# Kernel tuning notes

Hardware: AMD Instinct MI355X
Metric: run time of the kernel (lower is better)

## Reference

```python
import jax, jax.numpy as jnp
import numpy as np


def setup_inputs() -> dict:
    key = jax.random.key(0)
    k1, k2 = jax.random.split(key)
    B, H, W, D, C = 2, 128, 128, 128, 4
    image = jax.random.normal(k1, (B, H, W, D, C), dtype=jnp.float32)
    # multiplicative warp field in [0,1) keeps sample coords inside the volume
    transformation = jax.random.uniform(k2, (B, H, W, D, 3), dtype=jnp.float32)
    return {"image": image, "transformation": transformation}


def _make_grid(OH, OW, OD):
    # matches tf.meshgrid(x_lin, y_lin, z_lin) with default 'xy' indexing:
    # each output has shape (OH, OW, OD); stacked last-dim order (x, y, z)
    xl = jnp.linspace(-1.0, 1.0, OW)
    yl = jnp.linspace(-1.0, 1.0, OH)
    zl = jnp.linspace(-1.0, 1.0, OD)
    xc, yc, zc = jnp.meshgrid(xl, yl, zl, indexing="xy")
    return jnp.stack([xc, yc, zc], axis=-1)  # (OH, OW, OD, 3)


def _trilerp_one(img, coords):
    """img: (H, W, D, C); coords: (OH, OW, OD, 3) in [-1, 1]-style space."""
    H, W, D, C = img.shape
    x = 0.5 * (coords[..., 0] + 1.0) * W
    y = 0.5 * (coords[..., 1] + 1.0) * H
    z = 0.5 * (coords[..., 2] + 1.0) * D

    x0 = jnp.floor(x).astype(jnp.int32)
    y0 = jnp.floor(y).astype(jnp.int32)
    z0 = jnp.floor(z).astype(jnp.int32)
    x1 = jnp.clip(x0 + 1, 0, W - 1)
    y1 = jnp.clip(y0 + 1, 0, H - 1)
    z1 = jnp.clip(z0 + 1, 0, D - 1)
    x0 = jnp.clip(x0, 0, W - 1)
    y0 = jnp.clip(y0, 0, H - 1)
    z0 = jnp.clip(z0, 0, D - 1)

    # weights use the CLIPPED upper corners, as in the original
    dx = x1.astype(x.dtype) - x
    dy = y1.astype(y.dtype) - y
    dz = z1.astype(z.dtype) - z

    def g(yy, xx, zz):
        return img[yy, xx, zz]  # (OH, OW, OD, C) gather

    w = lambda a: a[..., None]
    out = (
        w(dz * dx * dy) * g(y0, x0, z0)
        + w(dz * dx * (1 - dy)) * g(y1, x0, z0)
        + w(dz * (1 - dx) * dy) * g(y0, x1, z0)
        + w(dz * (1 - dx) * (1 - dy)) * g(y1, x1, z0)
        + w((1 - dz) * dx * dy) * g(y0, x0, z1)
        + w((1 - dz) * dx * (1 - dy)) * g(y1, x0, z1)
        + w((1 - dz) * (1 - dx) * dy) * g(y0, x1, z1)
        + w((1 - dz) * (1 - dx) * (1 - dy)) * g(y1, x1, z1)
    )
    return out


def reference(image, transformation):
    # image: (B, H, W, D, C); transformation: (B, OH, OW, OD, 3)
    OH, OW, OD = transformation.shape[1:4]
    grid = _make_grid(OH, OW, OD)              # (OH, OW, OD, 3)
    coords = transformation * grid             # elementwise warp, as in source
    return jax.vmap(_trilerp_one, in_axes=(0, 0))(image, coords)
```

## Files before the change

kernel.cpp:

```cpp
#include <hip/hip_runtime.h>
#include <hip/hip_fp16.h>


typedef float f4 __attribute__((ext_vector_type(4)));
typedef unsigned int u32;
typedef u32 u4v __attribute__((ext_vector_type(4), aligned(8)));

__device__ inline float2 h2f(u32 b) {
    __half2 h = __builtin_bit_cast(__half2, b);
    return __half22float2(h);
}

__global__ __launch_bounds__(256) void cvt_kernel(
    const f4* __restrict__ img, uint2* __restrict__ himg)
{
    int idx = blockIdx.x * 256 + threadIdx.x;
    f4 v = img[idx];
    __half2 lo = __floats2half2_rn(v.x, v.y);
    __half2 hi = __floats2half2_rn(v.z, v.w);
    himg[idx] = make_uint2(__builtin_bit_cast(u32, lo), __builtin_bit_cast(u32, hi));
}

__global__ __launch_bounds__(256) void st3d_h_kernel(
    const u32* __restrict__ himg,
    const float* __restrict__ trans,
    f4* __restrict__ out)
{
    int bid = blockIdx.x;
    int q   = bid & 7;
    int n   = bid >> 3;
    int b   = n >> 10;
    int m   = ((n & 1023) << 8) | threadIdx.x;

    int kp = m & 63;
    int jp = (m >> 6) & 63;
    int ip = m >> 12;

    int qi = (q >> 2) & 1;
    int qj = (q >> 1) & 1;
    int qk = q & 1;

    int ipe = qi ? ip : (63 - ip);
    int i = (qi << 6) + ipe;
    int j = (qj << 6) + jp;
    int k = (qk << 6) + kp;

    int idx = (((b << 7) | i) << 14) | (j << 7) | k;

    const float step = 2.0f / 127.0f;
    float gx = -1.0f + step * (float)j;
    float gy = -1.0f + step * (float)i;
    float gz = -1.0f + step * (float)k;

    const float* t = trans + (size_t)idx * 3;
    float tx = __builtin_nontemporal_load(t + 0);
    float ty = __builtin_nontemporal_load(t + 1);
    float tz = __builtin_nontemporal_load(t + 2);

    float x = (tx * gx + 1.0f) * 64.0f;
    float y = (ty * gy + 1.0f) * 64.0f;
    float z = (tz * gz + 1.0f) * 64.0f;

    int x0 = (int)floorf(x);
    int y0 = (int)floorf(y);
    int z0 = (int)floorf(z);
    int x1 = min(max(x0 + 1, 0), 127);
    int y1 = min(max(y0 + 1, 0), 127);
    int z1 = min(max(z0 + 1, 0), 127);
    x0 = min(max(x0, 0), 127);
    y0 = min(max(y0, 0), 127);
    z0 = min(max(z0, 0), 127);

    float dx = (float)x1 - x;
    float dy = (float)y1 - y;
    float dz = (float)z1 - z;
    float ex = 1.0f - dx;
    float ey = 1.0f - dy;
    float ez = 1.0f - dz;

    int zb = min(z0, 126);
    int i0 = z0 - zb;
    int i1 = z1 - zb;

    int bb  = b << 21;
    int ry0 = bb + (y0 << 14);
    int ry1 = bb + (y1 << 14);
    int cx0 = x0 << 7;
    int cx1 = x1 << 7;

    const u4v* p0 = (const u4v*)(himg + (size_t)(ry0 + cx0 + zb) * 2);
    const u4v* p1 = (const u4v*)(himg + (size_t)(ry1 + cx0 + zb) * 2);
    const u4v* p2 = (const u4v*)(himg + (size_t)(ry0 + cx1 + zb) * 2);
    const u4v* p3 = (const u4v*)(himg + (size_t)(ry1 + cx1 + zb) * 2);

    u4v d0 = *p0;
    u4v d1 = *p1;
    u4v d2 = *p2;
    u4v d3 = *p3;

    float wA0 = dz * dx * dy, wB0 = ez * dx * dy;
    float wA1 = dz * dx * ey, wB1 = ez * dx * ey;
    float wA2 = dz * ex * dy, wB2 = ez * ex * dy;
    float wA3 = dz * ex * ey, wB3 = ez * ex * ey;

    float ox = 0.f, oy = 0.f, oz = 0.f, ow = 0.f;

#define ACC(d, wA, wB)                                            \
    {                                                             \
        u32 a0 = i0 ? (d).z : (d).x;               \
        u32 a1 = i0 ? (d).w : (d).y;               \
        u32 b0 = i1 ? (d).z : (d).x;               \
        u32 b1 = i1 ? (d).w : (d).y;               \
        float2 fa0 = h2f(a0), fa1 = h2f(a1);                      \
        float2 fb0 = h2f(b0), fb1 = h2f(b1);                      \
        ox += (wA) * fa0.x + (wB) * fb0.x;                        \
        oy += (wA) * fa0.y + (wB) * fb0.y;                        \
        oz += (wA) * fa1.x + (wB) * fb1.x;                        \
        ow += (wA) * fa1.y + (wB) * fb1.y;                        \
    }

    ACC(d0, wA0, wB0)
    ACC(d1, wA1, wB1)
    ACC(d2, wA2, wB2)
    ACC(d3, wA3, wB3)
#undef ACC

    f4 o = {ox, oy, oz, ow};
    __builtin_nontemporal_store(o, &out[idx]);
}

__global__ __launch_bounds__(256) void st3d_kernel(
    const float* __restrict__ img,
    const float* __restrict__ trans,
    f4* __restrict__ out)
{
    int bid = blockIdx.x;
    int q   = bid & 7;
    int n   = bid >> 3;
    int b   = n >> 10;
    int m   = ((n & 1023) << 8) | threadIdx.x;

    int kp = m & 63;
    int jp = (m >> 6) & 63;
    int ip = m >> 12;

    int qi = (q >> 2) & 1;
    int qj = (q >> 1) & 1;
    int qk = q & 1;

    int ipe = qi ? ip : (63 - ip);
    int i = (qi << 6) + ipe;
    int j = (qj << 6) + jp;
    int k = (qk << 6) + kp;

    int idx = (((b << 7) | i) << 14) | (j << 7) | k;

    const float step = 2.0f / 127.0f;
    float gx = -1.0f + step * (float)j;
    float gy = -1.0f + step * (float)i;
    float gz = -1.0f + step * (float)k;

    const float* t = trans + (size_t)idx * 3;
    float tx = __builtin_nontemporal_load(t + 0);
    float ty = __builtin_nontemporal_load(t + 1);
    float tz = __builtin_nontemporal_load(t + 2);

    float x = (tx * gx + 1.0f) * 64.0f;
    float y = (ty * gy + 1.0f) * 64.0f;
    float z = (tz * gz + 1.0f) * 64.0f;

    int x0 = (int)floorf(x);
    int y0 = (int)floorf(y);
    int z0 = (int)floorf(z);
    int x1 = min(max(x0 + 1, 0), 127);
    int y1 = min(max(y0 + 1, 0), 127);
    int z1 = min(max(z0 + 1, 0), 127);
    x0 = min(max(x0, 0), 127);
    y0 = min(max(y0, 0), 127);
    z0 = min(max(z0, 0), 127);

    float dx = (float)x1 - x;
    float dy = (float)y1 - y;
    float dz = (float)z1 - z;
    float ex = 1.0f - dx;
    float ey = 1.0f - dy;
    float ez = 1.0f - dz;

    const f4* img4 = (const f4*)img;
    int bb  = b << 21;
    int ry0 = bb + (y0 << 14);
    int ry1 = bb + (y1 << 14);
    int cx0 = x0 << 7;
    int cx1 = x1 << 7;

    int A0 = ry0 + cx0 + z0;
    int A1 = ry1 + cx0 + z0;
    int A2 = ry0 + cx1 + z0;
    int A3 = ry1 + cx1 + z0;
    int dzi = z1 - z0;

    f4 c000 = img4[A0];
    f4 c100 = img4[A1];
    f4 c010 = img4[A2];
    f4 c110 = img4[A3];
    f4 c001 = img4[A0 + dzi];
    f4 c101 = img4[A1 + dzi];
    f4 c011 = img4[A2 + dzi];
    f4 c111 = img4[A3 + dzi];

    float w000 = dz * dx * dy;
    float w100 = dz * dx * ey;
    float w010 = dz * ex * dy;
    float w110 = dz * ex * ey;
    float w001 = ez * dx * dy;
    float w101 = ez * dx * ey;
    float w011 = ez * ex * dy;
    float w111 = ez * ex * ey;

    f4 o = w000*c000 + w100*c100 + w010*c010 + w110*c110
         + w001*c001 + w101*c101 + w011*c011 + w111*c111;

    __builtin_nontemporal_store(o, &out[idx]);
}

extern "C" void kernel_launch(void* const* d_in, const int* in_sizes, int n_in,
                              void* d_out, int out_size, void* d_ws, size_t ws_size,
                              hipStream_t stream) {
    const float* img   = (const float*)d_in[0];
    const float* trans = (const float*)d_in[1];
    f4* out = (f4*)d_out;

    int N = in_sizes[1] / 3;
    int block = 256;
    int grid = N / block;

    size_t need = (size_t)N * 4 * sizeof(__half);
    if (ws_size >= need) {
        cvt_kernel<<<grid, block, 0, stream>>>((const f4*)img, (uint2*)d_ws);
        st3d_h_kernel<<<grid, block, 0, stream>>>((const u32*)d_ws, trans, out);
    } else {
        st3d_kernel<<<grid, block, 0, stream>>>(img, trans, out);
    }
}
```

Measured before the change: 237.6 us.

## Pre-pack 2x2x2 corner neighborhoods into 64-byte fp16 records for single-line gathers

A new conversion kernel writes, for each voxel, a record holding the fp16 values of its (y,x), (y+1,x), (y,x+1) and (y+1,x+1) neighbors. With the z pair adjacent, a sample's eight corners come from one contiguous 64-byte record instead of four scattered 16-byte loads. The sampling kernel also handles two output points per thread, halving the grid, to put more loads in flight. The cost is a 4x larger workspace and more write traffic in the conversion pass. The old half-precision path remains as a fallback when the workspace is too small.

```diff
diff --git a/kernel.cpp b/kernel.cpp
--- a/kernel.cpp
+++ b/kernel.cpp
@@ -9,6 +9,143 @@
 __device__ inline float2 h2f(u32 b) {
     __half2 h = __builtin_bit_cast(__half2, b);
     return __half22float2(h);
+}
+__device__ inline u32 f2h2(float a, float b) {
+    __half2 h = __floats2half2_rn(a, b);
+    return __builtin_bit_cast(u32, h);
+}
+
+__global__ __launch_bounds__(256) void cvtq_kernel(
+    const f4* __restrict__ img, u4v* __restrict__ rec)
+{
+    int t = blockIdx.x * 256 + threadIdx.x;
+    int z = t & 127;
+    int x = (t >> 7) & 127;
+    int y = (t >> 14) & 127;
+    int b = t >> 21;
+    int x1 = min(x + 1, 127);
+    int y1 = min(y + 1, 127);
+    int bb = b << 21;
+
+    f4 v00 = img[bb | (y  << 14) | (x  << 7) | z];
+    f4 v10 = img[bb | (y1 << 14) | (x  << 7) | z];
+    f4 v01 = img[bb | (y  << 14) | (x1 << 7) | z];
+    f4 v11 = img[bb | (y1 << 14) | (x1 << 7) | z];
+
+    u4v r0 = { f2h2(v00.x, v00.y), f2h2(v00.z, v00.w),
+               f2h2(v10.x, v10.y), f2h2(v10.z, v10.w) };
+    u4v r1 = { f2h2(v01.x, v01.y), f2h2(v01.z, v01.w),
+               f2h2(v11.x, v11.y), f2h2(v11.z, v11.w) };
+    rec[(size_t)t * 2]     = r0;
+    rec[(size_t)t * 2 + 1] = r1;
+}
+
+__global__ __launch_bounds__(256) void st3d_q_kernel(
+    const u32* __restrict__ rec,
+    const float* __restrict__ trans,
+    f4* __restrict__ out)
+{
+    int bid = blockIdx.x;
+    int q   = bid & 7;
+    int n   = bid >> 3;
+    int b   = n >> 9;
+    int mA  = ((n & 511) << 8) | threadIdx.x;
+    int mB  = mA + (1 << 17);
+
+    int qi = (q >> 2) & 1;
+    int qj = (q >> 1) & 1;
+    int qk = q & 1;
+
+    const float step = 2.0f / 127.0f;
+
+#define SETUPQ(S, mval)                                                    \
+    int kp##S  = (mval) & 63;                                              \
+    int jp##S  = ((mval) >> 6) & 63;                                       \
+    int ip##S  = (mval) >> 12;                                             \
+    int ipe##S = qi ? ip##S : (63 - ip##S);                                \
+    int i##S   = (qi << 6) + ipe##S;                                       \
+    int j##S   = (qj << 6) + jp##S;                                        \
+    int k##S   = (qk << 6) + kp##S;                                        \
+    int idx##S = (((b << 7) | i##S) << 14) | (j##S << 7) | k##S;           \
+    const float* t##S = trans + (size_t)idx##S * 3;                        \
+    float tx##S = __builtin_nontemporal_load(t##S + 0);                    \
+    float ty##S = __builtin_nontemporal_load(t##S + 1);                    \
+    float tz##S = __builtin_nontemporal_load(t##S + 2);
+
+    SETUPQ(A, mA)
+    SETUPQ(B, mB)
+
+#define GATHERQ(S)                                                         \
+    float gx##S = -1.0f + step * (float)j##S;                              \
+    float gy##S = -1.0f + step * (float)i##S;                              \
+    float gz##S = -1.0f + step * (float)k##S;                              \
+    float x##S = (tx##S * gx##S + 1.0f) * 64.0f;                           \
+    float y##S = (ty##S * gy##S + 1.0f) * 64.0f;                           \
+    float z##S = (tz##S * gz##S + 1.0f) * 64.0f;                           \
+    int x0##S = (int)floorf(x##S);                                         \
+    int y0##S = (int)floorf(y##S);                                         \
+    int z0##S = (int)floorf(z##S);                                         \
+    int x1##S = min(max(x0##S + 1, 0), 127);                               \
+    int y1##S = min(max(y0##S + 1, 0), 127);                               \
+    int z1##S = min(max(z0##S + 1, 0), 127);                               \
+    x0##S = min(max(x0##S, 0), 127);                                       \
+    y0##S = min(max(y0##S, 0), 127);                                       \
+    z0##S = min(max(z0##S, 0), 127);                                       \
+              \
+    float dx##S = (float)x1##S - x##S;                                     \
+    float dy##S = (float)y1##S - y##S;                                     \
+    float dz##S = (float)z1##S - z##S;                                     \
+    int zb##S = min(z0##S, 126);            \
+    int i0##S = z0##S - zb##S;             \
+    int i1##S = z1##S - zb##S;                             \
+    int r##S = (((b << 7) | y0##S) << 14) | (x0##S << 7) | zb##S;          \
+    const u4v* p##S = (const u4v*)(rec + (size_t)r##S * 8);                \
+    u4v L0##S = p##S[0];                       \
+    u4v L1##S = p##S[1];                       \
+    u4v L2##S = p##S[2];                       \
+    u4v L3##S = p##S[3];
+
+    GATHERQ(A)
+    GATHERQ(B)
+
+#define ACCQ(lo0, lo1, hi0, hi1, wA, wB)                                   \
+    {                                                                      \
+        u32 a0 = i0s ? (hi0) : (lo0);                       \
+        u32 a1 = i0s ? (hi1) : (lo1);                       \
+        u32 b0 = i1s ? (hi0) : (lo0);                       \
+        u32 b1 = i1s ? (hi1) : (lo1);                       \
+        float2 fa0 = h2f(a0), fa1 = h2f(a1);                               \
+        float2 fb0 = h2f(b0), fb1 = h2f(b1);                               \
+        ox += (wA) * fa0.x + (wB) * fb0.x;                                 \
+        oy += (wA) * fa0.y + (wB) * fb0.y;                                 \
+        oz += (wA) * fa1.x + (wB) * fb1.x;                                 \
+        ow += (wA) * fa1.y + (wB) * fb1.y;                                 \
+    }
+
+#define FINISHQ(S)                                                         \
+    {                                                                      \
+        float ex = 1.0f - dx##S, ey = 1.0f - dy##S, ez = 1.0f - dz##S;     \
+        float wA0 = dz##S * dx##S * dy##S, wB0 = ez * dx##S * dy##S;       \
+        float wA1 = dz##S * dx##S * ey,    wB1 = ez * dx##S * ey;          \
+        float wA2 = dz##S * ex * dy##S,    wB2 = ez * ex * dy##S;          \
+        float wA3 = dz##S * ex * ey,       wB3 = ez * ex * ey;             \
+        int i0s = i0##S, i1s = i1##S;                                      \
+        float ox = 0.f, oy = 0.f, oz = 0.f, ow = 0.f;                      \
+        ACCQ(L0##S.x, L0##S.y, L2##S.x, L2##S.y, wA0, wB0)    \
+        ACCQ(L0##S.z, L0##S.w, L2##S.z, L2##S.w, wA1, wB1)    \
+        ACCQ(L1##S.x, L1##S.y, L3##S.x, L3##S.y, wA2, wB2)    \
+        ACCQ(L1##S.z, L1##S.w, L3##S.z, L3##S.w, wA3, wB3)    \
+        f4 o = {ox, oy, oz, ow};                                           \
+        __builtin_nontemporal_store(o, &out[idx##S]);                      \
+    }
+
+    FINISHQ(A)
+    FINISHQ(B)
+
+#undef SETUPQ
+#undef GATHERQ
+#undef ACCQ
+#undef FINISHQ
 }
 
 __global__ __launch_bounds__(256) void cvt_kernel(
@@ -107,10 +244,10 @@
 
 #define ACC(d, wA, wB)                                            \
     {                                                             \
-        u32 a0 = i0 ? (d).z : (d).x;               \
-        u32 a1 = i0 ? (d).w : (d).y;               \
-        u32 b0 = i1 ? (d).z : (d).x;               \
-        u32 b1 = i1 ? (d).w : (d).y;               \
+        u32 a0 = i0 ? (d).z : (d).x;                              \
+        u32 a1 = i0 ? (d).w : (d).y;                              \
+        u32 b0 = i1 ? (d).z : (d).x;                              \
+        u32 b1 = i1 ? (d).w : (d).y;                              \
         float2 fa0 = h2f(a0), fa1 = h2f(a1);                      \
         float2 fb0 = h2f(b0), fb1 = h2f(b1);                      \
         ox += (wA) * fa0.x + (wB) * fb0.x;                        \
@@ -232,13 +369,19 @@
 
     int N = in_sizes[1] / 3;
     int block = 256;
-    int grid = N / block;
-
-    size_t need = (size_t)N * 4 * sizeof(__half);
-    if (ws_size >= need) {
-        cvt_kernel<<<grid, block, 0, stream>>>((const f4*)img, (uint2*)d_ws);
-        st3d_h_kernel<<<grid, block, 0, stream>>>((const u32*)d_ws, trans, out);
+
+    size_t need_q = (size_t)N * 32;
+    size_t need_h = (size_t)N * 8;
+
+    if (ws_size >= need_q) {
+        cvtq_kernel<<<N / block, block, 0, stream>>>((const f4*)img, (u4v*)d_ws);
+        st3d_q_kernel<<<N / (2 * block), block, 0, stream>>>(
+            (const u32*)d_ws, trans, out);
+    } else if (ws_size >= need_h) {
+        cvt_kernel<<<N / block, block, 0, stream>>>((const f4*)img, (uint2*)d_ws);
+        st3d_h_kernel<<<N / block, block, 0, stream>>>(
+            (const u32*)d_ws, trans, out);
     } else {
-        st3d_kernel<<<grid, block, 0, stream>>>(img, trans, out);
+        st3d_kernel<<<N / block, block, 0, stream>>>(img, trans, out);
     }
 }
```

After: 222.2 us, median of 2. -6.5%, faster.
